# Kernel tuning notes

Measured on AMD Instinct MI355X. Metric: run time of the kernel, lower is better.

## Reference

```python
import jax, jax.numpy as jnp
import numpy as np

RES = 16          # grid resolution per axis -> num_models = 4096
L_XYZ = 10        # xyz positional-encoding frequencies -> input_ch = 63
L_DIR = 4         # dir positional-encoding frequencies -> input_ch_views = 27
W = 32
N_RAYS, N_SAMPLES = 1024, 128
NM = RES * RES * RES


def _embed(x, L):
    # NeRF frequency encoding: [x, sin(2^k x), cos(2^k x)] for k in 0..L-1
    freqs = 2.0 ** jnp.arange(L, dtype=x.dtype)          # (L,)
    xf = x[..., None, :] * freqs[:, None]                # (N, L, 3)
    enc = jnp.concatenate([jnp.sin(xf), jnp.cos(xf)], axis=-1)
    return jnp.concatenate([x, enc.reshape(x.shape[0], -1)], axis=-1)


def setup_inputs() -> dict:
    key = jax.random.key(0)
    ks = jax.random.split(key, 16)
    s = 0.05
    pts = jax.random.uniform(ks[0], (N_RAYS, N_SAMPLES, 3), dtype=jnp.float32)
    vd = jax.random.normal(ks[1], (N_RAYS, 3), dtype=jnp.float32)
    vd = vd / jnp.linalg.norm(vd, axis=-1, keepdims=True)
    return {
        "pts": pts,
        "viewdirs": vd,
        "pts_w0": s * jax.random.normal(ks[2], (NM, W, 63), dtype=jnp.float32),
        "pts_b0": s * jax.random.normal(ks[3], (NM, W), dtype=jnp.float32),
        "pts_w1": s * jax.random.normal(ks[4], (NM, W, W), dtype=jnp.float32),
        "pts_b1": s * jax.random.normal(ks[5], (NM, W), dtype=jnp.float32),
        "feat_w": s * jax.random.normal(ks[6], (NM, W, W), dtype=jnp.float32),
        "feat_b": s * jax.random.normal(ks[7], (NM, W), dtype=jnp.float32),
        "sigma_w": s * jax.random.normal(ks[8], (NM, 1, W), dtype=jnp.float32),
        "sigma_b": s * jax.random.normal(ks[9], (NM, 1), dtype=jnp.float32),
        "view_w": s * jax.random.normal(ks[10], (NM, W, W + 27), dtype=jnp.float32),
        "view_b": s * jax.random.normal(ks[11], (NM, W), dtype=jnp.float32),
        "rgb_w": s * jax.random.normal(ks[12], (NM, 3, W), dtype=jnp.float32),
        "rgb_b": s * jax.random.normal(ks[13], (NM, 3), dtype=jnp.float32),
    }


def reference(pts, viewdirs, pts_w0, pts_b0, pts_w1, pts_b1, feat_w, feat_b,
              sigma_w, sigma_b, view_w, view_b, rgb_w, rgb_b):
    n_rays, n_samples, _ = pts.shape
    p = pts.reshape(-1, 3)                                        # (N, 3)
    v = jnp.broadcast_to(viewdirs[:, None, :],
                         (n_rays, n_samples, 3)).reshape(-1, 3)   # (N, 3)

    # voxel index (aabb = [0,1]^3)
    scaled = jnp.clip(p * RES, 0.0, RES - 1.0)
    i3 = scaled.astype(jnp.int32)
    idx = i3[:, 0] * (RES * RES) + i3[:, 1] * RES + i3[:, 2]      # (N,)

    ep = _embed(p, L_XYZ)                                         # (N, 63)
    ev = _embed(v, L_DIR)                                         # (N, 27)

    # per-point tiny MLP with gathered weights: h @ w^T + b
    h = jax.nn.relu(jnp.einsum('nd,nod->no', ep, pts_w0[idx]) + pts_b0[idx])
    h = jax.nn.relu(jnp.einsum('nd,nod->no', h, pts_w1[idx]) + pts_b1[idx])

    sigma = jnp.einsum('nd,nod->no', h, sigma_w[idx]) + sigma_b[idx]   # (N, 1)
    feat = jnp.einsum('nd,nod->no', h, feat_w[idx]) + feat_b[idx]      # (N, W)

    h2 = jnp.concatenate([feat, ev], axis=-1)                          # (N, W+27)
    h2 = jax.nn.relu(jnp.einsum('nd,nod->no', h2, view_w[idx]) + view_b[idx])
    rgb = jnp.einsum('nd,nod->no', h2, rgb_w[idx]) + rgb_b[idx]        # (N, 3)

    out = jnp.concatenate([rgb, sigma], axis=-1).reshape(n_rays, n_samples, 4)
    return out[..., :3], out[..., 3:4]
```

## Files before the change

kernel.cpp:

```cpp
#include <hip/hip_runtime.h>

#define NM    4096
#define NPTS  131072
#define CAP   128

typedef _Float16 h8 __attribute__((ext_vector_type(8)));
typedef _Float16 h2 __attribute__((ext_vector_type(2)));
typedef float    f4 __attribute__((ext_vector_type(4)));
typedef int      i4 __attribute__((ext_vector_type(4)));

#define MF(a, b, c) __builtin_amdgcn_mfma_f32_16x16x32_f16((a), (b), (c), 0, 0, 0)

#if __has_builtin(__builtin_amdgcn_global_load_lds)
#define USE_DMA 1
#else
#define USE_DMA 0
#endif

static __device__ inline h2 pk(float a, float b) {
    return __builtin_bit_cast(h2, __builtin_amdgcn_cvt_pkrtz(a, b));
}

static __device__ inline h8 pack8(float u0, float u1, float u2, float u3,
                                  float u4, float u5, float u6, float u7) {
    i4 t;
    t[0] = __builtin_bit_cast(int, pk(u0, u1));
    t[1] = __builtin_bit_cast(int, pk(u2, u3));
    t[2] = __builtin_bit_cast(int, pk(u4, u5));
    t[3] = __builtin_bit_cast(int, pk(u6, u7));
    return __builtin_bit_cast(h8, t);
}

static __device__ inline h8 lds_row8(const float* __restrict__ X, int base,
                                     int d0, int lim) {
    float u[8];
    #pragma unroll
    for (int jj = 0; jj < 8; jj++) {
        int d = d0 + jj;
        float raw = X[base + d];
        u[jj] = (d < lim) ? raw : 0.f;
    }
    return pack8(u[0], u[1], u[2], u[3], u[4], u[5], u[6], u[7]);
}

static __device__ inline h8 lds_row8a(const float* __restrict__ X, int off) {
    f4 v0 = *(const f4*)(X + off);
    f4 v1 = *(const f4*)(X + off + 4);
    return pack8(v0[0], v0[1], v0[2], v0[3], v1[0], v1[1], v1[2], v1[3]);
}

static __device__ inline h8 load_row8(const float* __restrict__ rb, int d0, int lim) {
    float u[8];
    #pragma unroll
    for (int jj = 0; jj < 8; jj++) {
        int d = d0 + jj;
        u[jj] = (d < lim) ? rb[d] : 0.f;
    }
    return pack8(u[0], u[1], u[2], u[3], u[4], u[5], u[6], u[7]);
}

static __device__ inline float encdim(int d, int lim, float x, float y, float z) {
    int tt = d - 3;
    int k  = tt / 6;
    int r  = tt - 6 * k;
    float p = x;
    p = (r == 1 || r == 4) ? y : p;
    p = (r == 2 || r == 5) ? z : p;
    float f   = __int_as_float((k + 127) << 23);
    float arg = p * f + ((r >= 3) ? 1.57079632679f : 0.f);
    float sv  = __sinf(arg);
    float raw = (d == 0) ? x : ((d == 1) ? y : z);
    float val = (d < 3) ? raw : sv;
    return (d < lim) ? val : 0.f;
}

static __device__ inline h8 makeB(f4 d0, f4 d1, int quad, int col) {
    int laneA = ((quad & 1) * 2) * 16 + col;
    int laneB = laneA + 16;
    float a0 = __shfl(d0[0], laneA), b0 = __shfl(d1[0], laneA);
    float a1 = __shfl(d0[1], laneA), b1 = __shfl(d1[1], laneA);
    float a2 = __shfl(d0[2], laneA), b2 = __shfl(d1[2], laneA);
    float a3 = __shfl(d0[3], laneA), b3 = __shfl(d1[3], laneA);
    float a4 = __shfl(d0[0], laneB), b4 = __shfl(d1[0], laneB);
    float a5 = __shfl(d0[1], laneB), b5 = __shfl(d1[1], laneB);
    float a6 = __shfl(d0[2], laneB), b6 = __shfl(d1[2], laneB);
    float a7 = __shfl(d0[3], laneB), b7 = __shfl(d1[3], laneB);
    bool hi = quad >= 2;
    return pack8(hi ? b0 : a0, hi ? b1 : a1, hi ? b2 : a2, hi ? b3 : a3,
                 hi ? b4 : a4, hi ? b5 : a5, hi ? b6 : a6, hi ? b7 : a7);
}

static __device__ inline f4 relu4(f4 a) {
    f4 r;
    r[0] = fmaxf(a[0], 0.f); r[1] = fmaxf(a[1], 0.f);
    r[2] = fmaxf(a[2], 0.f); r[3] = fmaxf(a[3], 0.f);
    return r;
}

#if USE_DMA
static __device__ inline void dma16(const float* g, const float* l) {
    __builtin_amdgcn_global_load_lds(
        (const __attribute__((address_space(1))) void*)g,
        (__attribute__((address_space(3))) void*)l, 16, 0, 0);
}
#endif

__global__ __launch_bounds__(256) void k_bucket(const float* __restrict__ pts,
                                                int* __restrict__ count,
                                                int* __restrict__ plist) {
    int n = blockIdx.x * 256 + threadIdx.x;
    if (n >= NPTS) return;
    float x = pts[3 * n + 0], y = pts[3 * n + 1], z = pts[3 * n + 2];
    int ix = (int)fminf(fmaxf(x * 16.f, 0.f), 15.f);
    int iy = (int)fminf(fmaxf(y * 16.f, 0.f), 15.f);
    int iz = (int)fminf(fmaxf(z * 16.f, 0.f), 15.f);
    int v = (ix << 8) | (iy << 4) | iz;
    int pos = atomicAdd(&count[v], 1);
    if (pos < CAP) plist[v * CAP + pos] = n;
}

__global__ __launch_bounds__(64) void k_mlp(
    const float* __restrict__ pts, const float* __restrict__ vds,
    const float* __restrict__ w0g, const float* __restrict__ b0g,
    const float* __restrict__ w1g, const float* __restrict__ b1g,
    const float* __restrict__ fwg, const float* __restrict__ fbg,
    const float* __restrict__ swg, const float* __restrict__ sbg,
    const float* __restrict__ vwg, const float* __restrict__ vbg,
    const float* __restrict__ rwg, const float* __restrict__ rbg,
    const int* __restrict__ count, const int* __restrict__ plist,
    float* __restrict__ out) {
    __shared__ __align__(16) float X[3040];

    const int v = blockIdx.x;
    const int t = threadIdx.x;
    const int c = min(count[v], CAP);
    if (c == 0) return;

    const int col  = t & 15;
    const int quad = t >> 4;
    const int k8   = quad * 8;

#if USE_DMA
    {
        const float* g = w0g + (size_t)v * 2016;
        #pragma unroll
        for (int k = 0; k < 7; k++) dma16(g + k * 256 + t * 4, X + k * 256);
        if (t < 56) dma16(g + 1792 + t * 4, X + 1792);
        g = w1g + (size_t)v * 1024;
        #pragma unroll
        for (int k = 0; k < 4; k++) dma16(g + k * 256 + t * 4, X + 2016 + k * 256);
    }
#endif

    float pxc, pyc, pzc, dxc, dyc, dzc;
    int ncur;
    {
        int sl = min(col, c - 1);
        ncur = plist[v * CAP + sl];
        pxc = pts[3 * ncur]; pyc = pts[3 * ncur + 1]; pzc = pts[3 * ncur + 2];
        int ray = ncur >> 7;
        dxc = vds[3 * ray]; dyc = vds[3 * ray + 1]; dzc = vds[3 * ray + 2];
    }
    f4 cB0[2], cB1[2], cFB[2], cVB[2];
    #pragma unroll
    for (int Ti = 0; Ti < 2; Ti++) {
        #pragma unroll
        for (int r = 0; r < 4; r++) {
            int row = Ti * 16 + quad * 4 + r;
            cB0[Ti][r] = b0g[v * 32 + row];
            cB1[Ti][r] = b1g[v * 32 + row];
            cFB[Ti][r] = fbg[v * 32 + row];
            cVB[Ti][r] = vbg[v * 32 + row];
        }
    }
    const float rb0 = rbg[v * 3 + 0], rb1 = rbg[v * 3 + 1], rb2 = rbg[v * 3 + 2];
    const float sb  = sbg[v];

    h8 aW0[2][2], aVW[2][2], aW1[2], aFW[2], aSG, aRGB;

#if USE_DMA
    __syncthreads();

    #pragma unroll
    for (int Ti = 0; Ti < 2; Ti++) {
        int rbase = (Ti * 16 + col) * 63;
        aW0[Ti][0] = lds_row8(X, rbase, k8, 63);
        aW0[Ti][1] = lds_row8(X, rbase, 32 + k8, 63);
        aW1[Ti] = lds_row8a(X, 2016 + (Ti * 16 + col) * 32 + k8);
    }
    __syncthreads();

    {
        const float* g = vwg + (size_t)v * 1888;
        #pragma unroll
        for (int k = 0; k < 7; k++) dma16(g + k * 256 + t * 4, X + k * 256);
        if (t < 24) dma16(g + 1792 + t * 4, X + 1792);
        g = fwg + (size_t)v * 1024;
        #pragma unroll
        for (int k = 0; k < 4; k++) dma16(g + k * 256 + t * 4, X + 1888 + k * 256);
        if (t < 8)  dma16(swg + (size_t)v * 32 + t * 4, X + 2912);
        if (t < 24) dma16(rwg + (size_t)v * 96 + t * 4, X + 2944);
    }
    __syncthreads();

    #pragma unroll
    for (int Ti = 0; Ti < 2; Ti++) {
        int rbase = (Ti * 16 + col) * 59;
        aVW[Ti][0] = lds_row8(X, rbase, k8, 59);
        aVW[Ti][1] = lds_row8(X, rbase, 32 + k8, 59);
        aFW[Ti] = lds_row8a(X, 1888 + (Ti * 16 + col) * 32 + k8);
    }
    aSG = (col == 0) ? lds_row8a(X, 2912 + k8) : h8{};
    aRGB = (col < 3) ? lds_row8a(X, 2944 + col * 32 + k8) : h8{};
#else
    #pragma unroll
    for (int Ti = 0; Ti < 2; Ti++) {
        const float* rb = w0g + (size_t)v * 2016 + (Ti * 16 + col) * 63;
        aW0[Ti][0] = load_row8(rb, k8, 63);
        aW0[Ti][1] = load_row8(rb, 32 + k8, 63);
        rb = vwg + (size_t)v * 1888 + (Ti * 16 + col) * 59;
        aVW[Ti][0] = load_row8(rb, k8, 59);
        aVW[Ti][1] = load_row8(rb, 32 + k8, 59);
        aW1[Ti] = load_row8(w1g + (size_t)v * 1024 + (Ti * 16 + col) * 32, k8, 32);
        aFW[Ti] = load_row8(fwg + (size_t)v * 1024 + (Ti * 16 + col) * 32, k8, 32);
    }
    aSG = (col == 0) ? load_row8(swg + (size_t)v * 32, k8, 32) : h8{};
    aRGB = (col < 3) ? load_row8(rwg + (size_t)v * 96 + col * 32, k8, 32) : h8{};
#endif

    const f4 z4 = {0.f, 0.f, 0.f, 0.f};

    for (int base = 0; base < c; base += 16) {
        const bool active = (base + col) < c;
        const int n = ncur;
        const float px = pxc, py = pyc, pz = pzc;
        const float dx = dxc, dy = dyc, dz = dzc;

        if (base + 16 < c) {
            int sl = min(base + 16 + col, c - 1);
            ncur = plist[v * CAP + sl];
            pxc = pts[3 * ncur]; pyc = pts[3 * ncur + 1]; pzc = pts[3 * ncur + 2];
            int ray = ncur >> 7;
            dxc = vds[3 * ray]; dyc = vds[3 * ray + 1]; dzc = vds[3 * ray + 2];
        }

        h8 bE0 = pack8(encdim(k8 + 0, 63, px, py, pz), encdim(k8 + 1, 63, px, py, pz),
                       encdim(k8 + 2, 63, px, py, pz), encdim(k8 + 3, 63, px, py, pz),
                       encdim(k8 + 4, 63, px, py, pz), encdim(k8 + 5, 63, px, py, pz),
                       encdim(k8 + 6, 63, px, py, pz), encdim(k8 + 7, 63, px, py, pz));
        h8 bE1 = pack8(encdim(32 + k8 + 0, 63, px, py, pz), encdim(32 + k8 + 1, 63, px, py, pz),
                       encdim(32 + k8 + 2, 63, px, py, pz), encdim(32 + k8 + 3, 63, px, py, pz),
                       encdim(32 + k8 + 4, 63, px, py, pz), encdim(32 + k8 + 5, 63, px, py, pz),
                       encdim(32 + k8 + 6, 63, px, py, pz), encdim(32 + k8 + 7, 63, px, py, pz));

        f4 d0 = MF(aW0[0][0], bE0, cB0[0]); d0 = MF(aW0[0][1], bE1, d0);
        f4 d1 = MF(aW0[1][0], bE0, cB0[1]); d1 = MF(aW0[1][1], bE1, d1);
        d0 = relu4(d0); d1 = relu4(d1);
        h8 bH = makeB(d0, d1, quad, col);

        f4 e0 = MF(aW1[0], bH, cB1[0]);
        f4 e1 = MF(aW1[1], bH, cB1[1]);
        e0 = relu4(e0); e1 = relu4(e1);
        h8 bG = makeB(e0, e1, quad, col);

        f4 s = MF(aSG, bG, z4);

        f4 f0 = MF(aFW[0], bG, cFB[0]);
        f4 f1 = MF(aFW[1], bG, cFB[1]);
        h8 bF = makeB(f0, f1, quad, col);

        h8 bD = pack8(encdim(k8 + 0, 27, dx, dy, dz), encdim(k8 + 1, 27, dx, dy, dz),
                      encdim(k8 + 2, 27, dx, dy, dz), encdim(k8 + 3, 27, dx, dy, dz),
                      encdim(k8 + 4, 27, dx, dy, dz), encdim(k8 + 5, 27, dx, dy, dz),
                      encdim(k8 + 6, 27, dx, dy, dz), encdim(k8 + 7, 27, dx, dy, dz));

        f4 v0 = MF(aVW[0][0], bF, cVB[0]); v0 = MF(aVW[0][1], bD, v0);
        f4 v1 = MF(aVW[1][0], bF, cVB[1]); v1 = MF(aVW[1][1], bD, v1);
        v0 = relu4(v0); v1 = relu4(v1);
        h8 bV = makeB(v0, v1, quad, col);

        f4 o = MF(aRGB, bV, z4);

        if (quad == 0 && active) {
            out[3 * n + 0] = o[0] + rb0;
            out[3 * n + 1] = o[1] + rb1;
            out[3 * n + 2] = o[2] + rb2;
            out[3 * NPTS + n] = s[0] + sb;
        }
    }
}

extern "C" void kernel_launch(void* const* d_in, const int* in_sizes, int n_in,
                              void* d_out, int out_size, void* d_ws, size_t ws_size,
                              hipStream_t stream) {
    const float* pts = (const float*)d_in[0];
    const float* vds = (const float*)d_in[1];
    const float* w0  = (const float*)d_in[2];
    const float* b0  = (const float*)d_in[3];
    const float* w1  = (const float*)d_in[4];
    const float* b1  = (const float*)d_in[5];
    const float* fw  = (const float*)d_in[6];
    const float* fb  = (const float*)d_in[7];
    const float* sw  = (const float*)d_in[8];
    const float* sb  = (const float*)d_in[9];
    const float* vw  = (const float*)d_in[10];
    const float* vb  = (const float*)d_in[11];
    const float* rw  = (const float*)d_in[12];
    const float* rb  = (const float*)d_in[13];
    float* out = (float*)d_out;

    int* count = (int*)d_ws;
    int* plist = (int*)((char*)d_ws + NM * sizeof(int));

    (void)hipMemsetAsync(count, 0, NM * sizeof(int), stream);
    k_bucket<<<NPTS / 256, 256, 0, stream>>>(pts, count, plist);
    k_mlp<<<NM, 64, 0, stream>>>(pts, vds, w0, b0, w1, b1, fw, fb, sw, sb,
                                 vw, vb, rw, rb, count, plist, out);
}
```

Before: 168.2 us.

## Use four waves per voxel block with split weight DMA and strided point tiles

The MLP kernel now runs 256 threads per voxel instead of one 64-lane wave. Each of the four waves DMAs a different weight matrix into a larger shared buffer, so all weights load in a single phase with one barrier instead of two serialized load phases. The waves then take 16-point tiles in turn with a stride of 64. This shortens the per-block load latency chain and spreads a voxel's points across waves. In exchange it doubles LDS use per block, and waves with no points sit idle through the DMA and then exit, since there are only about 32 points per voxel on average.

```diff
diff --git a/kernel.cpp b/kernel.cpp
--- a/kernel.cpp
+++ b/kernel.cpp
@@ -119,7 +119,7 @@
     if (pos < CAP) plist[v * CAP + pos] = n;
 }
 
-__global__ __launch_bounds__(64) void k_mlp(
+__global__ __launch_bounds__(256) void k_mlp(
     const float* __restrict__ pts, const float* __restrict__ vds,
     const float* __restrict__ w0g, const float* __restrict__ b0g,
     const float* __restrict__ w1g, const float* __restrict__ b1g,
@@ -129,89 +129,90 @@
     const float* __restrict__ rwg, const float* __restrict__ rbg,
     const int* __restrict__ count, const int* __restrict__ plist,
     float* __restrict__ out) {
-    __shared__ __align__(16) float X[3040];
+    __shared__ __align__(16) float X[6080];
 
     const int v = blockIdx.x;
     const int t = threadIdx.x;
     const int c = min(count[v], CAP);
     if (c == 0) return;
 
-    const int col  = t & 15;
-    const int quad = t >> 4;
+    const int wid  = t >> 6;
+    const int lane = t & 63;
+    const int col  = lane & 15;
+    const int quad = lane >> 4;
     const int k8   = quad * 8;
 
 #if USE_DMA
-    {
+    if (wid == 0) {
         const float* g = w0g + (size_t)v * 2016;
         #pragma unroll
-        for (int k = 0; k < 7; k++) dma16(g + k * 256 + t * 4, X + k * 256);
-        if (t < 56) dma16(g + 1792 + t * 4, X + 1792);
-        g = w1g + (size_t)v * 1024;
-        #pragma unroll
-        for (int k = 0; k < 4; k++) dma16(g + k * 256 + t * 4, X + 2016 + k * 256);
-    }
-#endif
+        for (int k = 0; k < 7; k++) dma16(g + k * 256 + lane * 4, X + k * 256);
+        if (lane < 56) dma16(g + 1792 + lane * 4, X + 1792);
+    } else if (wid == 1) {
+        const float* g = vwg + (size_t)v * 1888;
+        #pragma unroll
+        for (int k = 0; k < 7; k++) dma16(g + k * 256 + lane * 4, X + 3040 + k * 256);
+        if (lane < 24) dma16(g + 1792 + lane * 4, X + 4832);
+    } else if (wid == 2) {
+        const float* g = w1g + (size_t)v * 1024;
+        #pragma unroll
+        for (int k = 0; k < 4; k++) dma16(g + k * 256 + lane * 4, X + 2016 + k * 256);
+        if (lane < 8)  dma16(swg + (size_t)v * 32 + lane * 4, X + 5952);
+        if (lane < 24) dma16(rwg + (size_t)v * 96 + lane * 4, X + 5984);
+    } else {
+        const float* g = fwg + (size_t)v * 1024;
+        #pragma unroll
+        for (int k = 0; k < 4; k++) dma16(g + k * 256 + lane * 4, X + 4928 + k * 256);
+    }
+#endif
+
+    const bool hasWork = (wid * 16) < c;
 
     float pxc, pyc, pzc, dxc, dyc, dzc;
-    int ncur;
-    {
-        int sl = min(col, c - 1);
+    int ncur = 0;
+    f4 cB0[2], cB1[2], cFB[2], cVB[2];
+    float rb0 = 0.f, rb1 = 0.f, rb2 = 0.f, sb = 0.f;
+    if (hasWork) {
+        int sl = min(wid * 16 + col, c - 1);
         ncur = plist[v * CAP + sl];
         pxc = pts[3 * ncur]; pyc = pts[3 * ncur + 1]; pzc = pts[3 * ncur + 2];
         int ray = ncur >> 7;
         dxc = vds[3 * ray]; dyc = vds[3 * ray + 1]; dzc = vds[3 * ray + 2];
-    }
-    f4 cB0[2], cB1[2], cFB[2], cVB[2];
+        #pragma unroll
+        for (int Ti = 0; Ti < 2; Ti++) {
+            #pragma unroll
+            for (int r = 0; r < 4; r++) {
+                int row = Ti * 16 + quad * 4 + r;
+                cB0[Ti][r] = b0g[v * 32 + row];
+                cB1[Ti][r] = b1g[v * 32 + row];
+                cFB[Ti][r] = fbg[v * 32 + row];
+                cVB[Ti][r] = vbg[v * 32 + row];
+            }
+        }
+        rb0 = rbg[v * 3 + 0]; rb1 = rbg[v * 3 + 1]; rb2 = rbg[v * 3 + 2];
+        sb  = sbg[v];
+    }
+
+#if USE_DMA
+    __syncthreads();
+#endif
+    if (!hasWork) return;
+
+    h8 aW0[2][2], aVW[2][2], aW1[2], aFW[2], aSG, aRGB;
+#if USE_DMA
     #pragma unroll
     for (int Ti = 0; Ti < 2; Ti++) {
-        #pragma unroll
-        for (int r = 0; r < 4; r++) {
-            int row = Ti * 16 + quad * 4 + r;
-            cB0[Ti][r] = b0g[v * 32 + row];
-            cB1[Ti][r] = b1g[v * 32 + row];
-            cFB[Ti][r] = fbg[v * 32 + row];
-            cVB[Ti][r] = vbg[v * 32 + row];
-        }
-    }
-    const float rb0 = rbg[v * 3 + 0], rb1 = rbg[v * 3 + 1], rb2 = rbg[v * 3 + 2];
-    const float sb  = sbg[v];
-
-    h8 aW0[2][2], aVW[2][2], aW1[2], aFW[2], aSG, aRGB;
-
-#if USE_DMA
-    __syncthreads();
-
-    #pragma unroll
-    for (int Ti = 0; Ti < 2; Ti++) {
-        int rbase = (Ti * 16 + col) * 63;
-        aW0[Ti][0] = lds_row8(X, rbase, k8, 63);
-        aW0[Ti][1] = lds_row8(X, rbase, 32 + k8, 63);
+        int r0 = (Ti * 16 + col) * 63;
+        aW0[Ti][0] = lds_row8(X, r0, k8, 63);
+        aW0[Ti][1] = lds_row8(X, r0, 32 + k8, 63);
         aW1[Ti] = lds_row8a(X, 2016 + (Ti * 16 + col) * 32 + k8);
-    }
-    __syncthreads();
-
-    {
-        const float* g = vwg + (size_t)v * 1888;
-        #pragma unroll
-        for (int k = 0; k < 7; k++) dma16(g + k * 256 + t * 4, X + k * 256);
-        if (t < 24) dma16(g + 1792 + t * 4, X + 1792);
-        g = fwg + (size_t)v * 1024;
-        #pragma unroll
-        for (int k = 0; k < 4; k++) dma16(g + k * 256 + t * 4, X + 1888 + k * 256);
-        if (t < 8)  dma16(swg + (size_t)v * 32 + t * 4, X + 2912);
-        if (t < 24) dma16(rwg + (size_t)v * 96 + t * 4, X + 2944);
-    }
-    __syncthreads();
-
-    #pragma unroll
-    for (int Ti = 0; Ti < 2; Ti++) {
-        int rbase = (Ti * 16 + col) * 59;
-        aVW[Ti][0] = lds_row8(X, rbase, k8, 59);
-        aVW[Ti][1] = lds_row8(X, rbase, 32 + k8, 59);
-        aFW[Ti] = lds_row8a(X, 1888 + (Ti * 16 + col) * 32 + k8);
-    }
-    aSG = (col == 0) ? lds_row8a(X, 2912 + k8) : h8{};
-    aRGB = (col < 3) ? lds_row8a(X, 2944 + col * 32 + k8) : h8{};
+        int r1 = 3040 + (Ti * 16 + col) * 59;
+        aVW[Ti][0] = lds_row8(X, r1, k8, 59);
+        aVW[Ti][1] = lds_row8(X, r1, 32 + k8, 59);
+        aFW[Ti] = lds_row8a(X, 4928 + (Ti * 16 + col) * 32 + k8);
+    }
+    aSG  = (col == 0) ? lds_row8a(X, 5952 + k8) : h8{};
+    aRGB = (col < 3) ? lds_row8a(X, 5984 + col * 32 + k8) : h8{};
 #else
     #pragma unroll
     for (int Ti = 0; Ti < 2; Ti++) {
@@ -224,20 +225,20 @@
         aW1[Ti] = load_row8(w1g + (size_t)v * 1024 + (Ti * 16 + col) * 32, k8, 32);
         aFW[Ti] = load_row8(fwg + (size_t)v * 1024 + (Ti * 16 + col) * 32, k8, 32);
     }
-    aSG = (col == 0) ? load_row8(swg + (size_t)v * 32, k8, 32) : h8{};
+    aSG  = (col == 0) ? load_row8(swg + (size_t)v * 32, k8, 32) : h8{};
     aRGB = (col < 3) ? load_row8(rwg + (size_t)v * 96 + col * 32, k8, 32) : h8{};
 #endif
 
     const f4 z4 = {0.f, 0.f, 0.f, 0.f};
 
-    for (int base = 0; base < c; base += 16) {
+    for (int base = wid * 16; base < c; base += 64) {
         const bool active = (base + col) < c;
         const int n = ncur;
         const float px = pxc, py = pyc, pz = pzc;
         const float dx = dxc, dy = dyc, dz = dzc;
 
-        if (base + 16 < c) {
-            int sl = min(base + 16 + col, c - 1);
+        if (base + 64 < c) {
+            int sl = min(base + 64 + col, c - 1);
             ncur = plist[v * CAP + sl];
             pxc = pts[3 * ncur]; pyc = pts[3 * ncur + 1]; pzc = pts[3 * ncur + 2];
             int ray = ncur >> 7;
@@ -314,6 +315,6 @@
 
     (void)hipMemsetAsync(count, 0, NM * sizeof(int), stream);
     k_bucket<<<NPTS / 256, 256, 0, stream>>>(pts, count, plist);
-    k_mlp<<<NM, 64, 0, stream>>>(pts, vds, w0, b0, w1, b1, fw, fb, sw, sb,
-                                 vw, vb, rw, rb, count, plist, out);
-}
+    k_mlp<<<NM, 256, 0, stream>>>(pts, vds, w0, b0, w1, b1, fw, fb, sw, sb,
+                                  vw, vb, rw, rb, count, plist, out);
+}
```

Measured after the change: 176.9 us. 1.05x slower.

## Pack four voxels per block and overlap second weight DMA with first layers

Applied to the files above, without the earlier changes.

Each 256-thread block now handles four voxels, one per wavefront, each with its own LDS slice, so __syncthreads is replaced by per-wave waitcnt fences. The second weight batch (view, feat, sigma, rgb) is issued by DMA before layers 0-1 run on the first 16 points, hiding its latency behind compute, and positional encoding of the first chunk overlaps the first DMA. Bias loads are vectorised to float4. Risks include higher LDS use per block (48KB), which limits occupancy, and the removal of prefetching of the next chunk's points inside the loop.

```diff
diff --git a/kernel.cpp b/kernel.cpp
--- a/kernel.cpp
+++ b/kernel.cpp
@@ -119,7 +119,7 @@
     if (pos < CAP) plist[v * CAP + pos] = n;
 }
 
-__global__ __launch_bounds__(64) void k_mlp(
+__global__ __launch_bounds__(256) void k_mlp(
     const float* __restrict__ pts, const float* __restrict__ vds,
     const float* __restrict__ w0g, const float* __restrict__ b0g,
     const float* __restrict__ w1g, const float* __restrict__ b1g,
@@ -129,157 +129,186 @@
     const float* __restrict__ rwg, const float* __restrict__ rbg,
     const int* __restrict__ count, const int* __restrict__ plist,
     float* __restrict__ out) {
-    __shared__ __align__(16) float X[3040];
-
-    const int v = blockIdx.x;
-    const int t = threadIdx.x;
-    const int c = min(count[v], CAP);
+    __shared__ __align__(16) float X[4][3040];
+
+    const int t    = threadIdx.x;
+    const int wid  = t >> 6;
+    const int lane = t & 63;
+    const int col  = lane & 15;
+    const int quad = lane >> 4;
+    const int k8   = quad * 8;
+    const int v    = blockIdx.x * 4 + wid;
+    const int c    = min(count[v], CAP);
     if (c == 0) return;
-
-    const int col  = t & 15;
-    const int quad = t >> 4;
-    const int k8   = quad * 8;
+    float* Xw = X[wid];
 
 #if USE_DMA
     {
         const float* g = w0g + (size_t)v * 2016;
         #pragma unroll
-        for (int k = 0; k < 7; k++) dma16(g + k * 256 + t * 4, X + k * 256);
-        if (t < 56) dma16(g + 1792 + t * 4, X + 1792);
-        g = w1g + (size_t)v * 1024;
-        #pragma unroll
-        for (int k = 0; k < 4; k++) dma16(g + k * 256 + t * 4, X + 2016 + k * 256);
-    }
-#endif
-
-    float pxc, pyc, pzc, dxc, dyc, dzc;
-    int ncur;
-    {
-        int sl = min(col, c - 1);
-        ncur = plist[v * CAP + sl];
-        pxc = pts[3 * ncur]; pyc = pts[3 * ncur + 1]; pzc = pts[3 * ncur + 2];
-        int ray = ncur >> 7;
-        dxc = vds[3 * ray]; dyc = vds[3 * ray + 1]; dzc = vds[3 * ray + 2];
-    }
+        for (int k = 0; k < 7; k++) dma16(g + k * 256 + lane * 4, Xw + k * 256);
+        if (lane < 56) dma16(g + 1792 + lane * 4, Xw + 1792);
+        const float* g1 = w1g + (size_t)v * 1024;
+        #pragma unroll
+        for (int k = 0; k < 4; k++) dma16(g1 + k * 256 + lane * 4, Xw + 2016 + k * 256);
+    }
+#endif
+
+    int ncur = plist[v * CAP + min(col, c - 1)];
+    float px = pts[3 * ncur], py = pts[3 * ncur + 1], pz = pts[3 * ncur + 2];
+    int ray = ncur >> 7;
+    float dx = vds[3 * ray], dy = vds[3 * ray + 1], dz = vds[3 * ray + 2];
+
     f4 cB0[2], cB1[2], cFB[2], cVB[2];
     #pragma unroll
     for (int Ti = 0; Ti < 2; Ti++) {
-        #pragma unroll
-        for (int r = 0; r < 4; r++) {
-            int row = Ti * 16 + quad * 4 + r;
-            cB0[Ti][r] = b0g[v * 32 + row];
-            cB1[Ti][r] = b1g[v * 32 + row];
-            cFB[Ti][r] = fbg[v * 32 + row];
-            cVB[Ti][r] = vbg[v * 32 + row];
-        }
+        int ro = v * 32 + Ti * 16 + quad * 4;
+        cB0[Ti] = *(const f4*)(b0g + ro);
+        cB1[Ti] = *(const f4*)(b1g + ro);
+        cFB[Ti] = *(const f4*)(fbg + ro);
+        cVB[Ti] = *(const f4*)(vbg + ro);
     }
     const float rb0 = rbg[v * 3 + 0], rb1 = rbg[v * 3 + 1], rb2 = rbg[v * 3 + 2];
     const float sb  = sbg[v];
 
-    h8 aW0[2][2], aVW[2][2], aW1[2], aFW[2], aSG, aRGB;
+    h8 bE0, bE1, bD;
+    auto encode = [&](float qx, float qy, float qz, float ex, float ey, float ez) {
+        bE0 = pack8(encdim(k8 + 0, 63, qx, qy, qz), encdim(k8 + 1, 63, qx, qy, qz),
+                    encdim(k8 + 2, 63, qx, qy, qz), encdim(k8 + 3, 63, qx, qy, qz),
+                    encdim(k8 + 4, 63, qx, qy, qz), encdim(k8 + 5, 63, qx, qy, qz),
+                    encdim(k8 + 6, 63, qx, qy, qz), encdim(k8 + 7, 63, qx, qy, qz));
+        bE1 = pack8(encdim(32 + k8 + 0, 63, qx, qy, qz), encdim(32 + k8 + 1, 63, qx, qy, qz),
+                    encdim(32 + k8 + 2, 63, qx, qy, qz), encdim(32 + k8 + 3, 63, qx, qy, qz),
+                    encdim(32 + k8 + 4, 63, qx, qy, qz), encdim(32 + k8 + 5, 63, qx, qy, qz),
+                    encdim(32 + k8 + 6, 63, qx, qy, qz), encdim(32 + k8 + 7, 63, qx, qy, qz));
+        bD  = pack8(encdim(k8 + 0, 27, ex, ey, ez), encdim(k8 + 1, 27, ex, ey, ez),
+                    encdim(k8 + 2, 27, ex, ey, ez), encdim(k8 + 3, 27, ex, ey, ez),
+                    encdim(k8 + 4, 27, ex, ey, ez), encdim(k8 + 5, 27, ex, ey, ez),
+                    encdim(k8 + 6, 27, ex, ey, ez), encdim(k8 + 7, 27, ex, ey, ez));
+    };
+    encode(px, py, pz, dx, dy, dz);
+
+    h8 aW0[2][2], aW1[2], aVW[2][2], aFW[2], aSG, aRGB;
 
 #if USE_DMA
-    __syncthreads();
-
+    asm volatile("s_waitcnt vmcnt(0)" ::: "memory");
+    __builtin_amdgcn_sched_barrier(0);
     #pragma unroll
     for (int Ti = 0; Ti < 2; Ti++) {
-        int rbase = (Ti * 16 + col) * 63;
-        aW0[Ti][0] = lds_row8(X, rbase, k8, 63);
-        aW0[Ti][1] = lds_row8(X, rbase, 32 + k8, 63);
-        aW1[Ti] = lds_row8a(X, 2016 + (Ti * 16 + col) * 32 + k8);
-    }
-    __syncthreads();
+        int r0 = (Ti * 16 + col) * 63;
+        aW0[Ti][0] = lds_row8(Xw, r0, k8, 63);
+        aW0[Ti][1] = lds_row8(Xw, r0, 32 + k8, 63);
+        aW1[Ti] = lds_row8a(Xw, 2016 + (Ti * 16 + col) * 32 + k8);
+    }
+    asm volatile("s_waitcnt lgkmcnt(0)" ::: "memory");
+    __builtin_amdgcn_sched_barrier(0);
 
     {
         const float* g = vwg + (size_t)v * 1888;
         #pragma unroll
-        for (int k = 0; k < 7; k++) dma16(g + k * 256 + t * 4, X + k * 256);
-        if (t < 24) dma16(g + 1792 + t * 4, X + 1792);
-        g = fwg + (size_t)v * 1024;
-        #pragma unroll
-        for (int k = 0; k < 4; k++) dma16(g + k * 256 + t * 4, X + 1888 + k * 256);
-        if (t < 8)  dma16(swg + (size_t)v * 32 + t * 4, X + 2912);
-        if (t < 24) dma16(rwg + (size_t)v * 96 + t * 4, X + 2944);
-    }
-    __syncthreads();
-
+        for (int k = 0; k < 7; k++) dma16(g + k * 256 + lane * 4, Xw + k * 256);
+        if (lane < 24) dma16(g + 1792 + lane * 4, Xw + 1792);
+        const float* g1 = fwg + (size_t)v * 1024;
+        #pragma unroll
+        for (int k = 0; k < 4; k++) dma16(g1 + k * 256 + lane * 4, Xw + 1888 + k * 256);
+        if (lane < 8)  dma16(swg + (size_t)v * 32 + lane * 4, Xw + 2912);
+        if (lane < 24) dma16(rwg + (size_t)v * 96 + lane * 4, Xw + 2944);
+    }
+#else
+    {
+        #pragma unroll
+        for (int Ti = 0; Ti < 2; Ti++) {
+            const float* rb = w0g + (size_t)v * 2016 + (Ti * 16 + col) * 63;
+            aW0[Ti][0] = load_row8(rb, k8, 63);
+            aW0[Ti][1] = load_row8(rb, 32 + k8, 63);
+            aW1[Ti] = load_row8(w1g + (size_t)v * 1024 + (Ti * 16 + col) * 32, k8, 32);
+        }
+    }
+#endif
+
+    const f4 z4 = {0.f, 0.f, 0.f, 0.f};
+
+    f4 d0 = MF(aW0[0][0], bE0, cB0[0]); d0 = MF(aW0[0][1], bE1, d0);
+    f4 d1 = MF(aW0[1][0], bE0, cB0[1]); d1 = MF(aW0[1][1], bE1, d1);
+    d0 = relu4(d0); d1 = relu4(d1);
+    h8 bH = makeB(d0, d1, quad, col);
+    f4 e0 = MF(aW1[0], bH, cB1[0]);
+    f4 e1 = MF(aW1[1], bH, cB1[1]);
+    e0 = relu4(e0); e1 = relu4(e1);
+    h8 bG = makeB(e0, e1, quad, col);
+
+#if USE_DMA
+    asm volatile("s_waitcnt vmcnt(0)" ::: "memory");
+    __builtin_amdgcn_sched_barrier(0);
     #pragma unroll
     for (int Ti = 0; Ti < 2; Ti++) {
-        int rbase = (Ti * 16 + col) * 59;
-        aVW[Ti][0] = lds_row8(X, rbase, k8, 59);
-        aVW[Ti][1] = lds_row8(X, rbase, 32 + k8, 59);
-        aFW[Ti] = lds_row8a(X, 1888 + (Ti * 16 + col) * 32 + k8);
-    }
-    aSG = (col == 0) ? lds_row8a(X, 2912 + k8) : h8{};
-    aRGB = (col < 3) ? lds_row8a(X, 2944 + col * 32 + k8) : h8{};
+        int r1 = (Ti * 16 + col) * 59;
+        aVW[Ti][0] = lds_row8(Xw, r1, k8, 59);
+        aVW[Ti][1] = lds_row8(Xw, r1, 32 + k8, 59);
+        aFW[Ti] = lds_row8a(Xw, 1888 + (Ti * 16 + col) * 32 + k8);
+    }
+    aSG  = (col == 0) ? lds_row8a(Xw, 2912 + k8) : h8{};
+    aRGB = (col < 3) ? lds_row8a(Xw, 2944 + col * 32 + k8) : h8{};
 #else
-    #pragma unroll
-    for (int Ti = 0; Ti < 2; Ti++) {
-        const float* rb = w0g + (size_t)v * 2016 + (Ti * 16 + col) * 63;
-        aW0[Ti][0] = load_row8(rb, k8, 63);
-        aW0[Ti][1] = load_row8(rb, 32 + k8, 63);
-        rb = vwg + (size_t)v * 1888 + (Ti * 16 + col) * 59;
-        aVW[Ti][0] = load_row8(rb, k8, 59);
-        aVW[Ti][1] = load_row8(rb, 32 + k8, 59);
-        aW1[Ti] = load_row8(w1g + (size_t)v * 1024 + (Ti * 16 + col) * 32, k8, 32);
-        aFW[Ti] = load_row8(fwg + (size_t)v * 1024 + (Ti * 16 + col) * 32, k8, 32);
-    }
-    aSG = (col == 0) ? load_row8(swg + (size_t)v * 32, k8, 32) : h8{};
-    aRGB = (col < 3) ? load_row8(rwg + (size_t)v * 96 + col * 32, k8, 32) : h8{};
-#endif
-
-    const f4 z4 = {0.f, 0.f, 0.f, 0.f};
-
-    for (int base = 0; base < c; base += 16) {
-        const bool active = (base + col) < c;
-        const int n = ncur;
-        const float px = pxc, py = pyc, pz = pzc;
-        const float dx = dxc, dy = dyc, dz = dzc;
-
-        if (base + 16 < c) {
-            int sl = min(base + 16 + col, c - 1);
-            ncur = plist[v * CAP + sl];
-            pxc = pts[3 * ncur]; pyc = pts[3 * ncur + 1]; pzc = pts[3 * ncur + 2];
-            int ray = ncur >> 7;
-            dxc = vds[3 * ray]; dyc = vds[3 * ray + 1]; dzc = vds[3 * ray + 2];
+    {
+        #pragma unroll
+        for (int Ti = 0; Ti < 2; Ti++) {
+            const float* rb = vwg + (size_t)v * 1888 + (Ti * 16 + col) * 59;
+            aVW[Ti][0] = load_row8(rb, k8, 59);
+            aVW[Ti][1] = load_row8(rb, 32 + k8, 59);
+            aFW[Ti] = load_row8(fwg + (size_t)v * 1024 + (Ti * 16 + col) * 32, k8, 32);
         }
-
-        h8 bE0 = pack8(encdim(k8 + 0, 63, px, py, pz), encdim(k8 + 1, 63, px, py, pz),
-                       encdim(k8 + 2, 63, px, py, pz), encdim(k8 + 3, 63, px, py, pz),
-                       encdim(k8 + 4, 63, px, py, pz), encdim(k8 + 5, 63, px, py, pz),
-                       encdim(k8 + 6, 63, px, py, pz), encdim(k8 + 7, 63, px, py, pz));
-        h8 bE1 = pack8(encdim(32 + k8 + 0, 63, px, py, pz), encdim(32 + k8 + 1, 63, px, py, pz),
-                       encdim(32 + k8 + 2, 63, px, py, pz), encdim(32 + k8 + 3, 63, px, py, pz),
-                       encdim(32 + k8 + 4, 63, px, py, pz), encdim(32 + k8 + 5, 63, px, py, pz),
-                       encdim(32 + k8 + 6, 63, px, py, pz), encdim(32 + k8 + 7, 63, px, py, pz));
-
-        f4 d0 = MF(aW0[0][0], bE0, cB0[0]); d0 = MF(aW0[0][1], bE1, d0);
-        f4 d1 = MF(aW0[1][0], bE0, cB0[1]); d1 = MF(aW0[1][1], bE1, d1);
-        d0 = relu4(d0); d1 = relu4(d1);
-        h8 bH = makeB(d0, d1, quad, col);
-
-        f4 e0 = MF(aW1[0], bH, cB1[0]);
-        f4 e1 = MF(aW1[1], bH, cB1[1]);
-        e0 = relu4(e0); e1 = relu4(e1);
-        h8 bG = makeB(e0, e1, quad, col);
-
-        f4 s = MF(aSG, bG, z4);
-
+        aSG  = (col == 0) ? load_row8(swg + (size_t)v * 32, k8, 32) : h8{};
+        aRGB = (col < 3) ? load_row8(rwg + (size_t)v * 96 + col * 32, k8, 32) : h8{};
+    }
+#endif
+
+    {
+        f4 s  = MF(aSG, bG, z4);
         f4 f0 = MF(aFW[0], bG, cFB[0]);
         f4 f1 = MF(aFW[1], bG, cFB[1]);
         h8 bF = makeB(f0, f1, quad, col);
-
-        h8 bD = pack8(encdim(k8 + 0, 27, dx, dy, dz), encdim(k8 + 1, 27, dx, dy, dz),
-                      encdim(k8 + 2, 27, dx, dy, dz), encdim(k8 + 3, 27, dx, dy, dz),
-                      encdim(k8 + 4, 27, dx, dy, dz), encdim(k8 + 5, 27, dx, dy, dz),
-                      encdim(k8 + 6, 27, dx, dy, dz), encdim(k8 + 7, 27, dx, dy, dz));
-
         f4 v0 = MF(aVW[0][0], bF, cVB[0]); v0 = MF(aVW[0][1], bD, v0);
         f4 v1 = MF(aVW[1][0], bF, cVB[1]); v1 = MF(aVW[1][1], bD, v1);
         v0 = relu4(v0); v1 = relu4(v1);
         h8 bV = makeB(v0, v1, quad, col);
-
-        f4 o = MF(aRGB, bV, z4);
+        f4 o  = MF(aRGB, bV, z4);
+        if (quad == 0 && col < c) {
+            out[3 * ncur + 0] = o[0] + rb0;
+            out[3 * ncur + 1] = o[1] + rb1;
+            out[3 * ncur + 2] = o[2] + rb2;
+            out[3 * NPTS + ncur] = s[0] + sb;
+        }
+    }
+
+    for (int base = 16; base < c; base += 16) {
+        int n = plist[v * CAP + min(base + col, c - 1)];
+        const bool active = (base + col) < c;
+        float qx = pts[3 * n], qy = pts[3 * n + 1], qz = pts[3 * n + 2];
+        int r2 = n >> 7;
+        float ex = vds[3 * r2], ey = vds[3 * r2 + 1], ez = vds[3 * r2 + 2];
+        encode(qx, qy, qz, ex, ey, ez);
+
+        d0 = MF(aW0[0][0], bE0, cB0[0]); d0 = MF(aW0[0][1], bE1, d0);
+        d1 = MF(aW0[1][0], bE0, cB0[1]); d1 = MF(aW0[1][1], bE1, d1);
+        d0 = relu4(d0); d1 = relu4(d1);
+        bH = makeB(d0, d1, quad, col);
+
+        e0 = MF(aW1[0], bH, cB1[0]);
+        e1 = MF(aW1[1], bH, cB1[1]);
+        e0 = relu4(e0); e1 = relu4(e1);
+        bG = makeB(e0, e1, quad, col);
+
+        f4 s  = MF(aSG, bG, z4);
+        f4 f0 = MF(aFW[0], bG, cFB[0]);
+        f4 f1 = MF(aFW[1], bG, cFB[1]);
+        h8 bF = makeB(f0, f1, quad, col);
+
+        f4 v0 = MF(aVW[0][0], bF, cVB[0]); v0 = MF(aVW[0][1], bD, v0);
+        f4 v1 = MF(aVW[1][0], bF, cVB[1]); v1 = MF(aVW[1][1], bD, v1);
+        v0 = relu4(v0); v1 = relu4(v1);
+        h8 bV = makeB(v0, v1, quad, col);
+        f4 o  = MF(aRGB, bV, z4);
 
         if (quad == 0 && active) {
             out[3 * n + 0] = o[0] + rb0;
@@ -314,6 +343,6 @@
 
     (void)hipMemsetAsync(count, 0, NM * sizeof(int), stream);
     k_bucket<<<NPTS / 256, 256, 0, stream>>>(pts, count, plist);
-    k_mlp<<<NM, 64, 0, stream>>>(pts, vds, w0, b0, w1, b1, fw, fb, sw, sb,
-                                 vw, vb, rw, rb, count, plist, out);
-}
+    k_mlp<<<NM / 4, 256, 0, stream>>>(pts, vds, w0, b0, w1, b1, fw, fb, sw, sb,
+                                      vw, vb, rw, rb, count, plist, out);
+}
```

After: 169.4 us. No clear change (+0.7%).
